# Performance work log

Hardware: AMD Instinct MI355X
Metric: run time of the kernel (lower is better)

## Reference

```python
import jax, jax.numpy as jnp
import numpy as np

B, S, U = 64, 64, 16
EMB = 10
D = U - 2 + 2 * EMB      # encoder d_model = 34
DD = 3                   # decoder d_model
FF = 4                   # dim_feedforward
NL = 4                   # num layers (enc and dec)
ENH = 2                  # encoder heads
WV, SV = 10000, 400      # word / syllable vocab sizes


def _ln(x, w, b, eps=1e-5):
    mu = jnp.mean(x, -1, keepdims=True)
    var = jnp.mean((x - mu) ** 2, -1, keepdims=True)
    return (x - mu) / jnp.sqrt(var + eps) * w + b


def _mha(xq, xkv, qkv_w, qkv_b, out_w, out_b, nhead, mask=None):
    d = xq.shape[-1]
    wq, wk, wv = jnp.split(qkv_w, 3, axis=0)
    bq, bk, bv = jnp.split(qkv_b, 3, axis=0)
    q = xq @ wq.T + bq
    k = xkv @ wk.T + bk
    v = xkv @ wv.T + bv
    b_, sq, sk = q.shape[0], q.shape[1], k.shape[1]
    dh = d // nhead
    q = q.reshape(b_, sq, nhead, dh)
    k = k.reshape(b_, sk, nhead, dh)
    v = v.reshape(b_, sk, nhead, dh)
    scores = jnp.einsum('bqhd,bkhd->bhqk', q, k) * (1.0 / np.sqrt(dh))
    if mask is not None:
        scores = scores + mask
    attn = jax.nn.softmax(scores, axis=-1)
    out = jnp.einsum('bhqk,bkhd->bqhd', attn, v).reshape(b_, sq, d)
    return out @ out_w.T + out_b


def _pos_encoding(batch, d_model):
    # Faithful to the original quirk: pe has shape [max_len, 1, d] and is added
    # to a batch-first [B,S,D] tensor as x + pe[:B]  ->  row b of pe is added
    # to ALL sequence positions of batch element b.
    pos = jnp.arange(batch, dtype=jnp.float32)[:, None]
    div = jnp.exp(jnp.arange(0, d_model, 2, dtype=jnp.float32) * (-np.log(10000.0) / d_model))
    ang = pos * div  # [B, D/2]
    pe = jnp.stack([jnp.sin(ang), jnp.cos(ang)], axis=-1).reshape(batch, d_model)
    return pe[:, None, :]  # [B,1,D]


def setup_inputs() -> dict:
    key = jax.random.key(0)
    ks = iter(jax.random.split(key, 64))

    def n(shape, s=0.1):
        return jax.random.normal(next(ks), shape, dtype=jnp.float32) * s

    base = jax.random.uniform(next(ks), (B, S, U), dtype=jnp.float32)
    widx = jax.random.randint(next(ks), (B, S), 0, WV).astype(jnp.float32)
    sidx = jax.random.randint(next(ks), (B, S), 0, SV).astype(jnp.float32)
    src = base.at[:, :, U - 2].set(widx).at[:, :, U - 1].set(sidx)
    return {
        'src': src,
        'word_emb': jax.random.uniform(next(ks), (WV, EMB), jnp.float32, -0.1, 0.1),
        'syll_emb': jax.random.uniform(next(ks), (SV, EMB), jnp.float32, -0.1, 0.1),
        'enc_qkv_w': n((NL, 3 * D, D)), 'enc_qkv_b': jnp.zeros((NL, 3 * D)),
        'enc_out_w': n((NL, D, D)), 'enc_out_b': jnp.zeros((NL, D)),
        'enc_ln1_w': jnp.ones((NL, D)), 'enc_ln1_b': jnp.zeros((NL, D)),
        'enc_lin1_w': n((NL, FF, D)), 'enc_lin1_b': jnp.zeros((NL, FF)),
        'enc_lin2_w': n((NL, D, FF)), 'enc_lin2_b': jnp.zeros((NL, D)),
        'enc_ln2_w': jnp.ones((NL, D)), 'enc_ln2_b': jnp.zeros((NL, D)),
        'norm_w': jnp.ones((D,)), 'norm_b': jnp.zeros((D,)),
        'eo_w': jax.random.uniform(next(ks), (DD, D), jnp.float32, -0.1, 0.1),
        'eo_b': jnp.zeros((DD,)),
        'dec_sa_qkv_w': n((NL, 3 * DD, DD)), 'dec_sa_qkv_b': jnp.zeros((NL, 3 * DD)),
        'dec_sa_out_w': n((NL, DD, DD)), 'dec_sa_out_b': jnp.zeros((NL, DD)),
        'dec_ln1_w': jnp.ones((NL, DD)), 'dec_ln1_b': jnp.zeros((NL, DD)),
        'dec_ca_qkv_w': n((NL, 3 * DD, DD)), 'dec_ca_qkv_b': jnp.zeros((NL, 3 * DD)),
        'dec_ca_out_w': n((NL, DD, DD)), 'dec_ca_out_b': jnp.zeros((NL, DD)),
        'dec_ln2_w': jnp.ones((NL, DD)), 'dec_ln2_b': jnp.zeros((NL, DD)),
        'dec_lin1_w': n((NL, FF, DD)), 'dec_lin1_b': jnp.zeros((NL, FF)),
        'dec_lin2_w': n((NL, DD, FF)), 'dec_lin2_b': jnp.zeros((NL, DD)),
        'dec_ln3_w': jnp.ones((NL, DD)), 'dec_ln3_b': jnp.zeros((NL, DD)),
    }


def reference(src, word_emb, syll_emb,
              enc_qkv_w, enc_qkv_b, enc_out_w, enc_out_b,
              enc_ln1_w, enc_ln1_b, enc_lin1_w, enc_lin1_b,
              enc_lin2_w, enc_lin2_b, enc_ln2_w, enc_ln2_b,
              norm_w, norm_b, eo_w, eo_b,
              dec_sa_qkv_w, dec_sa_qkv_b, dec_sa_out_w, dec_sa_out_b,
              dec_ln1_w, dec_ln1_b,
              dec_ca_qkv_w, dec_ca_qkv_b, dec_ca_out_w, dec_ca_out_b,
              dec_ln2_w, dec_ln2_b,
              dec_lin1_w, dec_lin1_b, dec_lin2_w, dec_lin2_b,
              dec_ln3_w, dec_ln3_b):
    b, s = src.shape[0], src.shape[1]
    # embed_lyrics
    widx = src[:, :, U - 2].astype(jnp.int32)
    sidx = src[:, :, U - 1].astype(jnp.int32)
    x = jnp.concatenate([src[:, :, :U - 2], word_emb[widx], syll_emb[sidx]], axis=2)  # [B,S,D]
    x = x + _pos_encoding(b, D)
    # TransformerEncoder (post-norm, relu, dropout=0) + final LayerNorm
    for l in range(NL):
        sa = _mha(x, x, enc_qkv_w[l], enc_qkv_b[l], enc_out_w[l], enc_out_b[l], ENH)
        x = _ln(x + sa, enc_ln1_w[l], enc_ln1_b[l])
        ff = jax.nn.relu(x @ enc_lin1_w[l].T + enc_lin1_b[l]) @ enc_lin2_w[l].T + enc_lin2_b[l]
        x = _ln(x + ff, enc_ln2_w[l], enc_ln2_b[l])
    x = _ln(x, norm_w, norm_b)
    memory = x @ eo_w.T + eo_b  # [B,S,3]

    causal = jnp.where(jnp.tril(jnp.ones((s, s), bool)), 0.0, -1e9).astype(jnp.float32)

    def decode(tgt):
        y = tgt
        for l in range(NL):
            sa = _mha(y, y, dec_sa_qkv_w[l], dec_sa_qkv_b[l], dec_sa_out_w[l], dec_sa_out_b[l], 1, causal)
            y = _ln(y + sa, dec_ln1_w[l], dec_ln1_b[l])
            ca = _mha(y, memory, dec_ca_qkv_w[l], dec_ca_qkv_b[l], dec_ca_out_w[l], dec_ca_out_b[l], 1)
            y = _ln(y + ca, dec_ln2_w[l], dec_ln2_b[l])
            ff = jax.nn.relu(y @ dec_lin1_w[l].T + dec_lin1_b[l]) @ dec_lin2_w[l].T + dec_lin2_b[l]
            y = _ln(y + ff, dec_ln3_w[l], dec_ln3_b[l])
        return y

    # mask, position i only depends on tgt[:, :i+1], so a fixed-size padded
    # buffer + scan computes identical values.
    def step(tgt, i):
        out_i = jax.lax.dynamic_slice_in_dim(decode(tgt), i, 1, axis=1)  # [B,1,3]
        return jax.lax.dynamic_update_slice(tgt, out_i, (0, i + 1, 0)), None

    tgt0 = jnp.zeros((b, s, DD), jnp.float32)
    tgt, _ = jax.lax.scan(step, tgt0, jnp.arange(s - 1))
    return jnp.concatenate([tgt, src[:, :, U - 2:U - 1], src[:, :, U - 1:U]], axis=2)
```

## Files before the change

kernel.cpp:

```cpp
#include <hip/hip_runtime.h>
#include <math.h>

#define B_ 64
#define S_ 64
#define U_ 16
#define EMB_ 10
#define D_ 34
#define DD_ 3
#define FF_ 4
#define NL_ 4

typedef float v2f __attribute__((ext_vector_type(2)));

__global__ __launch_bounds__(512) void enc_kernel(
    const float* __restrict__ src, const float* __restrict__ wemb,
    const float* __restrict__ semb,
    const float* __restrict__ qkv_w, const float* __restrict__ qkv_b,
    const float* __restrict__ out_w, const float* __restrict__ out_b,
    const float* __restrict__ ln1_w, const float* __restrict__ ln1_b,
    const float* __restrict__ lin1_w, const float* __restrict__ lin1_b,
    const float* __restrict__ lin2_w, const float* __restrict__ lin2_b,
    const float* __restrict__ ln2_w, const float* __restrict__ ln2_b,
    const float* __restrict__ norm_w, const float* __restrict__ norm_b,
    const float* __restrict__ eo_w, const float* __restrict__ eo_b,
    float* __restrict__ mem, float* __restrict__ out)
{
    const int b = blockIdx.x;
    const int tid = threadIdx.x;
    const int wv_ = tid >> 6;
    const int lane = tid & 63;

    __shared__ float xs[S_][D_ + 1];
    __shared__ float tmp[S_][D_ + 1];
    __shared__ float att[S_][D_ + 1];
    __shared__ __align__(16) float qsh[2][S_][21];
    __shared__ __align__(16) float ksh[2][S_][20];
    __shared__ __align__(16) float vsh[2][S_][20];
    __shared__ float ffh[S_][5];
    __shared__ float pacc[4][128][19];

    const float rs17 = 0.24253562503633297f;
    const float negln = -logf(10000.0f) / (float)D_;

    #pragma unroll
    for (int rr = 0; rr < 5; ++rr) {
        int idx = tid + rr * 512;
        if (idx < S_ * D_) {
            int pos = idx / D_, d = idx % D_;
            float v;
            if (d < U_ - 2) {
                v = src[(b * S_ + pos) * U_ + d];
            } else if (d < U_ - 2 + EMB_) {
                int wi = (int)src[(b * S_ + pos) * U_ + (U_ - 2)];
                v = wemb[wi * EMB_ + (d - (U_ - 2))];
            } else {
                int si = (int)src[(b * S_ + pos) * U_ + (U_ - 1)];
                v = semb[si * EMB_ + (d - (U_ - 2 + EMB_))];
            }
            int k = d >> 1;
            float div = __expf((float)(2 * k) * negln);
            float ang = (float)b * div;
            v += (d & 1) ? __cosf(ang) : __sinf(ang);
            xs[pos][d] = v;
        }
    }
    __syncthreads();

    for (int l = 0; l < NL_; ++l) {
        const float* Wq = qkv_w + l * 3 * D_ * D_;
        const float* Bq = qkv_b + l * 3 * D_;

        {
            v2f xr2[17];
            #pragma unroll
            for (int d2 = 0; d2 < 17; ++d2) {
                v2f t; t.x = xs[lane][2 * d2]; t.y = xs[lane][2 * d2 + 1];
                xr2[d2] = t;
            }
            #pragma unroll
            for (int rb = 0; rb < 13; ++rb) {
                int r = wv_ + (rb << 3);
                if (r < 3 * D_) {
                    int ru = __builtin_amdgcn_readfirstlane(r);
                    const v2f* w2 = (const v2f*)(Wq + ru * D_);
                    v2f a2; a2.x = Bq[ru]; a2.y = 0.f;
                    #pragma unroll
                    for (int d2 = 0; d2 < 17; ++d2)
                        a2 = __builtin_elementwise_fma(xr2[d2], w2[d2], a2);
                    float acc = a2.x + a2.y;
                    if (ru < D_)          { int h = (ru >= 17), dd = ru - h * 17; qsh[h][lane][dd] = acc; }
                    else if (ru < 2 * D_) { int rr2 = ru - D_;     int h = (rr2 >= 17), dd = rr2 - h * 17; ksh[h][lane][dd] = acc; }
                    else                  { int rr2 = ru - 2 * D_; int h = (rr2 >= 17), dd = rr2 - h * 17; vsh[h][lane][dd] = acc; }
                }
            }
        }
        __syncthreads();

        {
            int c = tid >> 7, hq = tid & 127;
            int h = hq >> 6, qi = hq & 63;
            float qv[17], acc[17];
            #pragma unroll
            for (int d = 0; d < 17; ++d) { qv[d] = qsh[h][qi][d]; acc[d] = 0.f; }
            float ssum = 0.f;
            int j0 = c * 16;
            #pragma unroll 4
            for (int jj = 0; jj < 16; ++jj) {
                int j = j0 + jj;
                const float4* kr = (const float4*)ksh[h][j];
                const float4* vr = (const float4*)vsh[h][j];
                float4 k0 = kr[0], k1 = kr[1], k2 = kr[2], k3 = kr[3];
                float  k16 = ksh[h][j][16];
                float4 v0 = vr[0], v1 = vr[1], v2 = vr[2], v3 = vr[3];
                float  v16 = vsh[h][j][16];
                float sE = qv[0]*k0.x + qv[2]*k0.z + qv[4]*k1.x + qv[6]*k1.z +
                           qv[8]*k2.x + qv[10]*k2.z + qv[12]*k3.x + qv[14]*k3.z;
                float sO = qv[1]*k0.y + qv[3]*k0.w + qv[5]*k1.y + qv[7]*k1.w +
                           qv[9]*k2.y + qv[11]*k2.w + qv[13]*k3.y + qv[15]*k3.w;
                float sc = sE + sO + qv[16]*k16;
                float e = __expf(sc * rs17);
                ssum += e;
                acc[0] += e*v0.x;  acc[1] += e*v0.y;  acc[2] += e*v0.z;  acc[3] += e*v0.w;
                acc[4] += e*v1.x;  acc[5] += e*v1.y;  acc[6] += e*v1.z;  acc[7] += e*v1.w;
                acc[8] += e*v2.x;  acc[9] += e*v2.y;  acc[10] += e*v2.z; acc[11] += e*v2.w;
                acc[12] += e*v3.x; acc[13] += e*v3.y; acc[14] += e*v3.z; acc[15] += e*v3.w;
                acc[16] += e*v16;
            }
            #pragma unroll
            for (int d = 0; d < 17; ++d) pacc[c][hq][d] = acc[d];
            pacc[c][hq][17] = ssum;
        }
        __syncthreads();

        if (tid < 128) {
            int h = tid >> 6, qi = tid & 63;
            int off = h * 17;
            float ssum = pacc[0][tid][17] + pacc[1][tid][17] +
                         pacc[2][tid][17] + pacc[3][tid][17];
            float inv = 1.f / ssum;
            #pragma unroll
            for (int d = 0; d < 17; ++d)
                att[qi][off + d] = (pacc[0][tid][d] + pacc[1][tid][d] +
                                    pacc[2][tid][d] + pacc[3][tid][d]) * inv;
        }
        __syncthreads();

        {
            v2f ar2[17];
            #pragma unroll
            for (int d2 = 0; d2 < 17; ++d2) {
                v2f t; t.x = att[lane][2 * d2]; t.y = att[lane][2 * d2 + 1];
                ar2[d2] = t;
            }
            const float* Wo = out_w + l * D_ * D_;
            const float* Bo = out_b + l * D_;
            #pragma unroll
            for (int rb = 0; rb < 5; ++rb) {
                int d = wv_ + (rb << 3);
                if (d < D_) {
                    int du = __builtin_amdgcn_readfirstlane(d);
                    const v2f* w2 = (const v2f*)(Wo + du * D_);
                    v2f a2; a2.x = Bo[du]; a2.y = 0.f;
                    #pragma unroll
                    for (int d2 = 0; d2 < 17; ++d2)
                        a2 = __builtin_elementwise_fma(ar2[d2], w2[d2], a2);
                    tmp[lane][du] = xs[lane][du] + a2.x + a2.y;
                }
            }
        }
        __syncthreads();

        {
            int row = tid >> 3, sub = tid & 7;
            float s = 0.f, sq = 0.f;
            #pragma unroll
            for (int d = sub; d < D_; d += 8) { float t = tmp[row][d]; s += t; sq = fmaf(t, t, sq); }
            #pragma unroll
            for (int m = 1; m < 8; m <<= 1) { s += __shfl_xor(s, m, 8); sq += __shfl_xor(sq, m, 8); }
            float mu = s * (1.0f / D_);
            float var = fmaf(sq, 1.0f / D_, -mu * mu);
            float rstd = rsqrtf(var + 1e-5f);
            #pragma unroll
            for (int d = sub; d < D_; d += 8)
                xs[row][d] = (tmp[row][d] - mu) * rstd * ln1_w[l * D_ + d] + ln1_b[l * D_ + d];
        }
        __syncthreads();

        if (wv_ < 4) {
            int fu = __builtin_amdgcn_readfirstlane(wv_);
            const v2f* w2 = (const v2f*)(lin1_w + l * FF_ * D_ + fu * D_);
            v2f a2; a2.x = lin1_b[l * FF_ + fu]; a2.y = 0.f;
            #pragma unroll
            for (int d2 = 0; d2 < 17; ++d2) {
                v2f t; t.x = xs[lane][2 * d2]; t.y = xs[lane][2 * d2 + 1];
                a2 = __builtin_elementwise_fma(t, w2[d2], a2);
            }
            ffh[lane][fu] = fmaxf(a2.x + a2.y, 0.f);
        }
        __syncthreads();

        {
            float h0 = ffh[lane][0], h1 = ffh[lane][1],
                  h2 = ffh[lane][2], h3 = ffh[lane][3];
            const float* W2 = lin2_w + l * D_ * FF_;
            const float* B2 = lin2_b + l * D_;
            #pragma unroll
            for (int rb = 0; rb < 5; ++rb) {
                int d = wv_ + (rb << 3);
                if (d < D_) {
                    int du = __builtin_amdgcn_readfirstlane(d);
                    const float* wrow = W2 + du * FF_;
                    float acc = fmaf(h0, wrow[0], fmaf(h1, wrow[1],
                                fmaf(h2, wrow[2], fmaf(h3, wrow[3], B2[du]))));
                    tmp[lane][du] = xs[lane][du] + acc;
                }
            }
        }
        __syncthreads();

        {
            int row = tid >> 3, sub = tid & 7;
            float s = 0.f, sq = 0.f;
            #pragma unroll
            for (int d = sub; d < D_; d += 8) { float t = tmp[row][d]; s += t; sq = fmaf(t, t, sq); }
            #pragma unroll
            for (int m = 1; m < 8; m <<= 1) { s += __shfl_xor(s, m, 8); sq += __shfl_xor(sq, m, 8); }
            float mu = s * (1.0f / D_);
            float var = fmaf(sq, 1.0f / D_, -mu * mu);
            float rstd = rsqrtf(var + 1e-5f);
            #pragma unroll
            for (int d = sub; d < D_; d += 8)
                xs[row][d] = (tmp[row][d] - mu) * rstd * ln2_w[l * D_ + d] + ln2_b[l * D_ + d];
        }
        __syncthreads();
    }

    {
        int row = tid >> 3, sub = tid & 7;
        float s = 0.f, sq = 0.f;
        #pragma unroll
        for (int d = sub; d < D_; d += 8) { float t = xs[row][d]; s += t; sq = fmaf(t, t, sq); }
        #pragma unroll
        for (int m = 1; m < 8; m <<= 1) { s += __shfl_xor(s, m, 8); sq += __shfl_xor(sq, m, 8); }
        float mu = s * (1.0f / D_);
        float var = fmaf(sq, 1.0f / D_, -mu * mu);
        float rstd = rsqrtf(var + 1e-5f);
        #pragma unroll
        for (int d = sub; d < D_; d += 8)
            tmp[row][d] = (xs[row][d] - mu) * rstd * norm_w[d] + norm_b[d];
    }
    __syncthreads();

    if (wv_ < 3) {
        int ru = __builtin_amdgcn_readfirstlane(wv_);
        const v2f* w2 = (const v2f*)(eo_w + ru * D_);
        v2f a2; a2.x = eo_b[ru]; a2.y = 0.f;
        #pragma unroll
        for (int d2 = 0; d2 < 17; ++d2) {
            v2f t; t.x = tmp[lane][2 * d2]; t.y = tmp[lane][2 * d2 + 1];
            a2 = __builtin_elementwise_fma(t, w2[d2], a2);
        }
        mem[(b * S_ + lane) * DD_ + ru] = a2.x + a2.y;
    }

    if (tid < S_) {
        out[(b * S_ + tid) * 5 + 3] = src[(b * S_ + tid) * U_ + (U_ - 2)];
        out[(b * S_ + tid) * 5 + 4] = src[(b * S_ + tid) * U_ + (U_ - 1)];
    }
}

#define PIN(x) asm volatile("" : "+v"(x))

template <int N> struct IC { static constexpr int value = N; };

template <int CTRL>
__device__ __forceinline__ float dpp_add(float v) {
    int t = __builtin_amdgcn_update_dpp(0, __float_as_int(v), CTRL, 0xf, 0xf, true);
    return v + __int_as_float(t);
}

__device__ __forceinline__ float red16(float v) {
    v = dpp_add<0x111>(v);
    v = dpp_add<0x112>(v);
    v = dpp_add<0x114>(v);
    v = dpp_add<0x118>(v);
    return v;
}

template <int L>
__device__ __forceinline__ float rlane(float v) {
    return __int_as_float(__builtin_amdgcn_readlane(__float_as_int(v), L));
}

__device__ __forceinline__ void ln3e(float z0, float z1, float z2,
                                     float w0, float w1, float w2,
                                     float b0, float b1, float b2,
                                     float& o0, float& o1, float& o2) {
    float s1 = (z0 + z1) + z2;
    float s2 = fmaf(z0, z0, fmaf(z1, z1, z2 * z2));
    float mu = s1 * (1.0f / 3.0f);
    float vpe = fmaf(s2, (1.0f / 3.0f), fmaf(-mu, mu, 1e-5f));
    float rstd = __builtin_amdgcn_rsqf(vpe);
    o0 = fmaf(z0 - mu, rstd * w0, b0);
    o1 = fmaf(z1 - mu, rstd * w1, b1);
    o2 = fmaf(z2 - mu, rstd * w2, b2);
}

__global__ __launch_bounds__(64, 1) void dec_kernel(
    const float* __restrict__ mem,
    const float* __restrict__ sa_qkv_w, const float* __restrict__ sa_qkv_b,
    const float* __restrict__ sa_out_w, const float* __restrict__ sa_out_b,
    const float* __restrict__ gln1_w, const float* __restrict__ gln1_b,
    const float* __restrict__ ca_qkv_w, const float* __restrict__ ca_qkv_b,
    const float* __restrict__ ca_out_w, const float* __restrict__ ca_out_b,
    const float* __restrict__ gln2_w, const float* __restrict__ gln2_b,
    const float* __restrict__ l1_w, const float* __restrict__ l1_b,
    const float* __restrict__ l2_w, const float* __restrict__ l2_b,
    const float* __restrict__ gln3_w, const float* __restrict__ gln3_b,
    float* __restrict__ out)
{
    const int b = blockIdx.x;
    const int lane = threadIdx.x;
    const float LOG2E = 1.4426950408889634f;
    const float rs3 = 0.5773502691896258f;
    const float QS = rs3 * LOG2E;

    __shared__ __align__(16) float fst[NL_][40];
    for (int t = lane; t < NL_ * 40; t += 64) {
        int l = t / 40, s = t % 40;
        float v = 0.f;
        if      (s < 12) v = l1_w[l * 12 + s] * gln2_w[l * 3 + (s % 3)];
        else if (s < 16) {
            int j = s - 12;
            v = l1_w[l * 12 + j * 3 + 0] * gln2_b[l * 3 + 0] +
                l1_w[l * 12 + j * 3 + 1] * gln2_b[l * 3 + 1] +
                l1_w[l * 12 + j * 3 + 2] * gln2_b[l * 3 + 2] + l1_b[l * 4 + j];
        }
        else if (s < 28) v = l2_w[l * 12 + (s - 16)];
        else if (s < 31) v = l2_b[l * 3 + (s - 28)];
        else if (s < 34) v = gln3_w[l * 3 + (s - 31)];
        else if (s < 37) v = gln3_b[l * 3 + (s - 34)];
        fst[l][s] = v;
    }
    __syncthreads();

    float Wsq[NL_][9][3], Bsq[NL_][9];
    float Wso[NL_][3][3], Bso[NL_][3];
    float N1w[NL_][3], N1b[NL_][3];
    float N2w[NL_][3], N2b[NL_][3];
    float Bco[NL_][3];
    float wcu[NL_][3];
    float swcu[NL_];
    float cbb[NL_];
    float cvp[NL_][3];

    #pragma unroll
    for (int l = 0; l < NL_; ++l) {
        #pragma unroll
        for (int r = 0; r < 9; ++r) {
            float sc = (r < 3) ? QS : 1.0f;
            Bsq[l][r] = sa_qkv_b[l * 9 + r] * sc;
            #pragma unroll
            for (int c = 0; c < 3; ++c) Wsq[l][r][c] = sa_qkv_w[l * 27 + r * 3 + c] * sc;
        }
        #pragma unroll
        for (int r = 0; r < 3; ++r) {
            Bso[l][r] = sa_out_b[l * 3 + r];
            Bco[l][r] = ca_out_b[l * 3 + r];
            N1w[l][r] = gln1_w[l * 3 + r];  N1b[l][r] = gln1_b[l * 3 + r];
            N2w[l][r] = gln2_w[l * 3 + r];  N2b[l][r] = gln2_b[l * 3 + r];
            #pragma unroll
            for (int c = 0; c < 3; ++c) Wso[l][r][c] = sa_out_w[l * 9 + r * 3 + c];
        }
    }

    float m0 = mem[(b * S_ + lane) * DD_ + 0];
    float m1 = mem[(b * S_ + lane) * DD_ + 1];
    float m2 = mem[(b * S_ + lane) * DD_ + 2];

    #pragma unroll
    for (int l = 0; l < NL_; ++l) {
        float ck[3], cv[3], cuv[3];
        #pragma unroll
        for (int r = 0; r < 3; ++r) {
            ck[r] = ca_qkv_w[l * 27 + (3 + r) * 3 + 0] * m0 +
                    ca_qkv_w[l * 27 + (3 + r) * 3 + 1] * m1 +
                    ca_qkv_w[l * 27 + (3 + r) * 3 + 2] * m2 + ca_qkv_b[l * 9 + 3 + r];
            cv[r] = ca_qkv_w[l * 27 + (6 + r) * 3 + 0] * m0 +
                    ca_qkv_w[l * 27 + (6 + r) * 3 + 1] * m1 +
                    ca_qkv_w[l * 27 + (6 + r) * 3 + 2] * m2 + ca_qkv_b[l * 9 + 6 + r];
        }
        #pragma unroll
        for (int s = 0; s < 3; ++s)
            cuv[s] = QS * (ca_qkv_w[l * 27 + 0 + s] * ck[0] +
                           ca_qkv_w[l * 27 + 3 + s] * ck[1] +
                           ca_qkv_w[l * 27 + 6 + s] * ck[2]);
        float cbv = QS * (ca_qkv_b[l * 9 + 0] * ck[0] +
                          ca_qkv_b[l * 9 + 1] * ck[1] +
                          ca_qkv_b[l * 9 + 2] * ck[2]);
        #pragma unroll
        for (int r = 0; r < 3; ++r)
            cvp[l][r] = ca_out_w[l * 9 + r * 3 + 0] * cv[0] +
                        ca_out_w[l * 9 + r * 3 + 1] * cv[1] +
                        ca_out_w[l * 9 + r * 3 + 2] * cv[2];
        #pragma unroll
        for (int r = 0; r < 3; ++r) wcu[l][r] = cuv[r] * N1w[l][r];
        swcu[l] = wcu[l][0] + wcu[l][1] + wcu[l][2];
        cbb[l]  = cbv + cuv[0] * N1b[l][0] + cuv[1] * N1b[l][1] + cuv[2] * N1b[l][2];
    }

    #pragma unroll
    for (int l = 0; l < NL_; ++l) {
        #pragma unroll
        for (int r = 0; r < 9; ++r) {
            PIN(Bsq[l][r]);
            #pragma unroll
            for (int c = 0; c < 3; ++c) PIN(Wsq[l][r][c]);
        }
        PIN(swcu[l]); PIN(cbb[l]);
        #pragma unroll
        for (int r = 0; r < 3; ++r) {
            PIN(Bso[l][r]); PIN(Bco[l][r]);
            PIN(N1w[l][r]); PIN(N1b[l][r]); PIN(N2w[l][r]); PIN(N2b[l][r]);
            PIN(wcu[l][r]); PIN(cvp[l][r]);
            #pragma unroll
            for (int c = 0; c < 3; ++c) PIN(Wso[l][r][c]);
        }
    }

    float sk[NL_][3] = {{0.f}}, sv[NL_][3] = {{0.f}};

    if (lane < 3) out[(b * S_ + 0) * 5 + lane] = 0.f;

    float y0 = 0.f, y1 = 0.f, y2 = 0.f;

    auto run_range = [&](int ibeg, int iend, auto nstc) {
        constexpr int NST = decltype(nstc)::value;
        constexpr int RL = (NST == 4) ? 15 : (NST == 5) ? 31 : 63;
        for (int i = ibeg; i < iend; ++i) {
            float msa = (lane <= i) ? 0.f : -1.0e30f;
            bool isme = (lane == i);
            #pragma unroll
            for (int l = 0; l < NL_; ++l) {
                float wv[40];
                {
                    const float4* fp = (const float4*)fst[l];
                    #pragma unroll
                    for (int k = 0; k < 10; ++k) {
                        float4 t4 = fp[k];
                        wv[4 * k + 0] = t4.x; wv[4 * k + 1] = t4.y;
                        wv[4 * k + 2] = t4.z; wv[4 * k + 3] = t4.w;
                    }
                }

                float q[3], kn[3], vn[3], vp[3];
                #pragma unroll
                for (int r = 0; r < 3; ++r) {
                    kn[r] = fmaf(Wsq[l][3 + r][0], y0, fmaf(Wsq[l][3 + r][1], y1, fmaf(Wsq[l][3 + r][2], y2, Bsq[l][3 + r])));
                    q[r]  = fmaf(Wsq[l][r][0], y0, fmaf(Wsq[l][r][1], y1, fmaf(Wsq[l][r][2], y2, Bsq[l][r])));
                    vn[r] = fmaf(Wsq[l][6 + r][0], y0, fmaf(Wsq[l][6 + r][1], y1, fmaf(Wsq[l][6 + r][2], y2, Bsq[l][6 + r])));
                }
                #pragma unroll
                for (int r = 0; r < 3; ++r)
                    vp[r] = fmaf(Wso[l][r][0], vn[0], fmaf(Wso[l][r][1], vn[1], Wso[l][r][2] * vn[2]));
                if (isme) {
                    #pragma unroll
                    for (int r = 0; r < 3; ++r) { sk[l][r] = kn[r]; sv[l][r] = vp[r]; }
                }
                float sc = fmaf(q[0], sk[l][0], fmaf(q[1], sk[l][1], fmaf(q[2], sk[l][2], msa)));
                float e = __builtin_amdgcn_exp2f(sc);
                float se  = red16(e);
                float sa0 = red16(e * sv[l][0]);
                float sa1 = red16(e * sv[l][1]);
                float sa2 = red16(e * sv[l][2]);
                if constexpr (NST >= 5) {
                    se  = dpp_add<0x142>(se);  sa0 = dpp_add<0x142>(sa0);
                    sa1 = dpp_add<0x142>(sa1); sa2 = dpp_add<0x142>(sa2);
                }
                if constexpr (NST >= 6) {
                    se  = dpp_add<0x143>(se);  sa0 = dpp_add<0x143>(sa0);
                    sa1 = dpp_add<0x143>(sa1); sa2 = dpp_add<0x143>(sa2);
                }
                float yb0 = y0 + Bso[l][0], yb1 = y1 + Bso[l][1], yb2 = y2 + Bso[l][2];
                float es = rlane<RL>(se);
                float S0 = rlane<RL>(sa0), S1 = rlane<RL>(sa1), S2 = rlane<RL>(sa2);
                float inv = __builtin_amdgcn_rcpf(es);
                float z0 = fmaf(S0, inv, yb0), z1 = fmaf(S1, inv, yb1), z2v = fmaf(S2, inv, yb2);

                float s1m = (z0 + z1) + z2v;
                float mu = s1m * (1.0f / 3.0f);
                float zw = fmaf(z0, wcu[l][0], fmaf(z1, wcu[l][1], z2v * wcu[l][2]));
                float inner = fmaf(-mu, swcu[l], zw);
                float s2m = fmaf(z0, z0, fmaf(z1, z1, z2v * z2v));
                float vpe = fmaf(s2m, (1.0f / 3.0f), fmaf(-mu, mu, 1e-5f));
                float rstd1 = __builtin_amdgcn_rsqf(vpe);
                float sc2 = fmaf(rstd1, inner, cbb[l]);
                float e2 = __builtin_amdgcn_exp2f(sc2);
                float ce  = red16(e2);
                float ca0 = red16(e2 * cvp[l][0]);
                float ca1 = red16(e2 * cvp[l][1]);
                float ca2 = red16(e2 * cvp[l][2]);
                ce  = dpp_add<0x142>(ce);  ca0 = dpp_add<0x142>(ca0);
                ca1 = dpp_add<0x142>(ca1); ca2 = dpp_add<0x142>(ca2);
                ce  = dpp_add<0x143>(ce);  ca0 = dpp_add<0x143>(ca0);
                ca1 = dpp_add<0x143>(ca1); ca2 = dpp_add<0x143>(ca2);
                float y1_0 = fmaf(z0 - mu, rstd1 * N1w[l][0], N1b[l][0]);
                float y1_1 = fmaf(z1 - mu, rstd1 * N1w[l][1], N1b[l][1]);
                float y1_2 = fmaf(z2v - mu, rstd1 * N1w[l][2], N1b[l][2]);
                float yc0 = y1_0 + Bco[l][0], yc1 = y1_1 + Bco[l][1], yc2 = y1_2 + Bco[l][2];
                float cs = rlane<63>(ce);
                float C0 = rlane<63>(ca0), C1 = rlane<63>(ca1), C2 = rlane<63>(ca2);
                float inv2 = __builtin_amdgcn_rcpf(cs);
                float g0 = fmaf(C0, inv2, yc0), g1 = fmaf(C1, inv2, yc1), g2 = fmaf(C2, inv2, yc2);

                float t1m = (g0 + g1) + g2;
                float mu2 = t1m * (1.0f / 3.0f);
                float c20 = g0 - mu2, c21 = g1 - mu2, c22 = g2 - mu2;
                float t2m = fmaf(g0, g0, fmaf(g1, g1, g2 * g2));
                float vpe2 = fmaf(t2m, (1.0f / 3.0f), fmaf(-mu2, mu2, 1e-5f));
                float rstd2 = __builtin_amdgcn_rsqf(vpe2);
                #pragma unroll
                for (int k = 0; k < 37; ++k) PIN(wv[k]);
                float d0 = fmaf(wv[0], c20, fmaf(wv[1],  c21, wv[2]  * c22));
                float d1 = fmaf(wv[3], c20, fmaf(wv[4],  c21, wv[5]  * c22));
                float d2 = fmaf(wv[6], c20, fmaf(wv[7],  c21, wv[8]  * c22));
                float d3 = fmaf(wv[9], c20, fmaf(wv[10], c21, wv[11] * c22));
                float h0 = fmaxf(fmaf(rstd2, d0, wv[12]), 0.f);
                float h1 = fmaxf(fmaf(rstd2, d1, wv[13]), 0.f);
                float h2 = fmaxf(fmaf(rstd2, d2, wv[14]), 0.f);
                float h3 = fmaxf(fmaf(rstd2, d3, wv[15]), 0.f);
                float y2_0 = fmaf(c20, rstd2 * N2w[l][0], N2b[l][0]);
                float y2_1 = fmaf(c21, rstd2 * N2w[l][1], N2b[l][1]);
                float y2_2 = fmaf(c22, rstd2 * N2w[l][2], N2b[l][2]);
                float yf0 = y2_0 + wv[28], yf1 = y2_1 + wv[29], yf2 = y2_2 + wv[30];
                float f0 = fmaf(wv[16], h0, fmaf(wv[17], h1, fmaf(wv[18], h2, fmaf(wv[19], h3, yf0))));
                float f1 = fmaf(wv[20], h0, fmaf(wv[21], h1, fmaf(wv[22], h2, fmaf(wv[23], h3, yf1))));
                float f2 = fmaf(wv[24], h0, fmaf(wv[25], h1, fmaf(wv[26], h2, fmaf(wv[27], h3, yf2))));
                ln3e(f0, f1, f2,
                     wv[31], wv[32], wv[33], wv[34], wv[35], wv[36],
                     y0, y1, y2);
            }
            if (lane == 0) {
                out[(b * S_ + i + 1) * 5 + 0] = y0;
                out[(b * S_ + i + 1) * 5 + 1] = y1;
                out[(b * S_ + i + 1) * 5 + 2] = y2;
            }
        }
    };

    run_range(0, 15, IC<4>{});
    run_range(15, 31, IC<5>{});
    run_range(31, S_ - 1, IC<6>{});
}

extern "C" void kernel_launch(void* const* d_in, const int* in_sizes, int n_in,
                              void* d_out, int out_size, void* d_ws, size_t ws_size,
                              hipStream_t stream) {
    const float* src  = (const float*)d_in[0];
    const float* wemb = (const float*)d_in[1];
    const float* semb = (const float*)d_in[2];

    float* mem = (float*)d_ws;
    float* out = (float*)d_out;

    enc_kernel<<<B_, 512, 0, stream>>>(
        src, wemb, semb,
        (const float*)d_in[3],  (const float*)d_in[4],
        (const float*)d_in[5],  (const float*)d_in[6],
        (const float*)d_in[7],  (const float*)d_in[8],
        (const float*)d_in[9],  (const float*)d_in[10],
        (const float*)d_in[11], (const float*)d_in[12],
        (const float*)d_in[13], (const float*)d_in[14],
        (const float*)d_in[15], (const float*)d_in[16],
        (const float*)d_in[17], (const float*)d_in[18],
        mem, out);

    dec_kernel<<<B_, 64, 0, stream>>>(
        mem,
        (const float*)d_in[19], (const float*)d_in[20],
        (const float*)d_in[21], (const float*)d_in[22],
        (const float*)d_in[23], (const float*)d_in[24],
        (const float*)d_in[25], (const float*)d_in[26],
        (const float*)d_in[27], (const float*)d_in[28],
        (const float*)d_in[29], (const float*)d_in[30],
        (const float*)d_in[31], (const float*)d_in[32],
        (const float*)d_in[33], (const float*)d_in[34],
        (const float*)d_in[35], (const float*)d_in[36],
        out);
}
```

Measured before the change: 316.2 us.

## Interleave two batch elements per decoder wave with butterfly reductions and rcp-free softmax

Each decoder wave now processes two batch elements at once, interleaving their serial dependency chains to hide latency, and the grid is halved. Lane reductions switch from row-shift DPP plus readlane to a full butterfly (DPP, permlane16/32 swap) so every lane holds the sum. The softmax normalisation is folded into the layer norm by scaling the residual by the sum and scaling epsilon by its square, which removes the reciprocal. The fixed-range prefix reductions are replaced by full 64-lane reductions every step, and register pressure doubles.

Result: slower. 517.3 us (+63.6%).

```diff
diff --git a/kernel.cpp b/kernel.cpp
--- a/kernel.cpp
+++ b/kernel.cpp
@@ -11,6 +11,7 @@
 #define NL_ 4
 
 typedef float v2f __attribute__((ext_vector_type(2)));
+typedef unsigned uint2v __attribute__((ext_vector_type(2)));
 
 __global__ __launch_bounds__(512) void enc_kernel(
     const float* __restrict__ src, const float* __restrict__ wemb,
@@ -271,25 +272,37 @@
 
 #define PIN(x) asm volatile("" : "+v"(x))
 
-template <int N> struct IC { static constexpr int value = N; };
-
 template <int CTRL>
 __device__ __forceinline__ float dpp_add(float v) {
     int t = __builtin_amdgcn_update_dpp(0, __float_as_int(v), CTRL, 0xf, 0xf, true);
     return v + __int_as_float(t);
 }
 
-__device__ __forceinline__ float red16(float v) {
-    v = dpp_add<0x111>(v);
-    v = dpp_add<0x112>(v);
-    v = dpp_add<0x114>(v);
-    v = dpp_add<0x118>(v);
+__device__ __forceinline__ float bfly_sum(float v) {
+    v = dpp_add<0xB1>(v);
+    v = dpp_add<0x4E>(v);
+    v = dpp_add<0x124>(v);
+    v = dpp_add<0x128>(v);
+#if __has_builtin(__builtin_amdgcn_permlane16_swap)
+    {
+        uint2v p = __builtin_amdgcn_permlane16_swap(__float_as_uint(v), __float_as_uint(v), false, false);
+        v = __uint_as_float(p.x) + __uint_as_float(p.y);
+    }
+#else
+    v += __uint_as_float(__builtin_amdgcn_ds_swizzle(__float_as_int(v), 0x401F));
+#endif
+#if __has_builtin(__builtin_amdgcn_permlane32_swap)
+    {
+        uint2v p = __builtin_amdgcn_permlane32_swap(__float_as_uint(v), __float_as_uint(v), false, false);
+        v = __uint_as_float(p.x) + __uint_as_float(p.y);
+    }
+#else
+    {
+        int ix = (((int)threadIdx.x & 63) ^ 32) << 2;
+        v += __uint_as_float(__builtin_amdgcn_ds_bpermute(ix, __float_as_int(v)));
+    }
+#endif
     return v;
-}
-
-template <int L>
-__device__ __forceinline__ float rlane(float v) {
-    return __int_as_float(__builtin_amdgcn_readlane(__float_as_int(v), L));
 }
 
 __device__ __forceinline__ void ln3e(float z0, float z1, float z2,
@@ -319,7 +332,7 @@
     const float* __restrict__ gln3_w, const float* __restrict__ gln3_b,
     float* __restrict__ out)
 {
-    const int b = blockIdx.x;
+    const int b0 = blockIdx.x * 2;
     const int lane = threadIdx.x;
     const float LOG2E = 1.4426950408889634f;
     const float rs3 = 0.5773502691896258f;
@@ -349,10 +362,10 @@
     float N1w[NL_][3], N1b[NL_][3];
     float N2w[NL_][3], N2b[NL_][3];
     float Bco[NL_][3];
-    float wcu[NL_][3];
-    float swcu[NL_];
-    float cbb[NL_];
-    float cvp[NL_][3];
+    float wcu[2][NL_][3];
+    float swcu[2][NL_];
+    float cbb[2][NL_];
+    float cvp[2][NL_][3];
 
     #pragma unroll
     for (int l = 0; l < NL_; ++l) {
@@ -374,84 +387,95 @@
         }
     }
 
-    float m0 = mem[(b * S_ + lane) * DD_ + 0];
-    float m1 = mem[(b * S_ + lane) * DD_ + 1];
-    float m2 = mem[(b * S_ + lane) * DD_ + 2];
+    #pragma unroll
+    for (int u = 0; u < 2; ++u) {
+        int bb = b0 + u;
+        float m0 = mem[(bb * S_ + lane) * DD_ + 0];
+        float m1 = mem[(bb * S_ + lane) * DD_ + 1];
+        float m2 = mem[(bb * S_ + lane) * DD_ + 2];
+        #pragma unroll
+        for (int l = 0; l < NL_; ++l) {
+            float ck[3], cv[3], cuv[3];
+            #pragma unroll
+            for (int r = 0; r < 3; ++r) {
+                ck[r] = ca_qkv_w[l * 27 + (3 + r) * 3 + 0] * m0 +
+                        ca_qkv_w[l * 27 + (3 + r) * 3 + 1] * m1 +
+                        ca_qkv_w[l * 27 + (3 + r) * 3 + 2] * m2 + ca_qkv_b[l * 9 + 3 + r];
+                cv[r] = ca_qkv_w[l * 27 + (6 + r) * 3 + 0] * m0 +
+                        ca_qkv_w[l * 27 + (6 + r) * 3 + 1] * m1 +
+                        ca_qkv_w[l * 27 + (6 + r) * 3 + 2] * m2 + ca_qkv_b[l * 9 + 6 + r];
+            }
+            #pragma unroll
+            for (int s = 0; s < 3; ++s)
+                cuv[s] = QS * (ca_qkv_w[l * 27 + 0 + s] * ck[0] +
+                               ca_qkv_w[l * 27 + 3 + s] * ck[1] +
+                               ca_qkv_w[l * 27 + 6 + s] * ck[2]);
+            float cbv = QS * (ca_qkv_b[l * 9 + 0] * ck[0] +
+                              ca_qkv_b[l * 9 + 1] * ck[1] +
+                              ca_qkv_b[l * 9 + 2] * ck[2]);
+            #pragma unroll
+            for (int r = 0; r < 3; ++r)
+                cvp[u][l][r] = ca_out_w[l * 9 + r * 3 + 0] * cv[0] +
+                               ca_out_w[l * 9 + r * 3 + 1] * cv[1] +
+                               ca_out_w[l * 9 + r * 3 + 2] * cv[2];
+            #pragma unroll
+            for (int r = 0; r < 3; ++r) wcu[u][l][r] = cuv[r] * N1w[l][r];
+            swcu[u][l] = wcu[u][l][0] + wcu[u][l][1] + wcu[u][l][2];
+            cbb[u][l]  = cbv + cuv[0] * N1b[l][0] + cuv[1] * N1b[l][1] + cuv[2] * N1b[l][2];
+        }
+    }
 
     #pragma unroll
     for (int l = 0; l < NL_; ++l) {
-        float ck[3], cv[3], cuv[3];
-        #pragma unroll
-        for (int r = 0; r < 3; ++r) {
-            ck[r] = ca_qkv_w[l * 27 + (3 + r) * 3 + 0] * m0 +
-                    ca_qkv_w[l * 27 + (3 + r) * 3 + 1] * m1 +
-                    ca_qkv_w[l * 27 + (3 + r) * 3 + 2] * m2 + ca_qkv_b[l * 9 + 3 + r];
-            cv[r] = ca_qkv_w[l * 27 + (6 + r) * 3 + 0] * m0 +
-                    ca_qkv_w[l * 27 + (6 + r) * 3 + 1] * m1 +
-                    ca_qkv_w[l * 27 + (6 + r) * 3 + 2] * m2 + ca_qkv_b[l * 9 + 6 + r];
-        }
-        #pragma unroll
-        for (int s = 0; s < 3; ++s)
-            cuv[s] = QS * (ca_qkv_w[l * 27 + 0 + s] * ck[0] +
-                           ca_qkv_w[l * 27 + 3 + s] * ck[1] +
-                           ca_qkv_w[l * 27 + 6 + s] * ck[2]);
-        float cbv = QS * (ca_qkv_b[l * 9 + 0] * ck[0] +
-                          ca_qkv_b[l * 9 + 1] * ck[1] +
-                          ca_qkv_b[l * 9 + 2] * ck[2]);
-        #pragma unroll
-        for (int r = 0; r < 3; ++r)
-            cvp[l][r] = ca_out_w[l * 9 + r * 3 + 0] * cv[0] +
-                        ca_out_w[l * 9 + r * 3 + 1] * cv[1] +
-                        ca_out_w[l * 9 + r * 3 + 2] * cv[2];
-        #pragma unroll
-        for (int r = 0; r < 3; ++r) wcu[l][r] = cuv[r] * N1w[l][r];
-        swcu[l] = wcu[l][0] + wcu[l][1] + wcu[l][2];
-        cbb[l]  = cbv + cuv[0] * N1b[l][0] + cuv[1] * N1b[l][1] + cuv[2] * N1b[l][2];
-    }
-
-    #pragma unroll
-    for (int l = 0; l < NL_; ++l) {
         #pragma unroll
         for (int r = 0; r < 9; ++r) {
             PIN(Bsq[l][r]);
             #pragma unroll
             for (int c = 0; c < 3; ++c) PIN(Wsq[l][r][c]);
         }
-        PIN(swcu[l]); PIN(cbb[l]);
         #pragma unroll
         for (int r = 0; r < 3; ++r) {
             PIN(Bso[l][r]); PIN(Bco[l][r]);
             PIN(N1w[l][r]); PIN(N1b[l][r]); PIN(N2w[l][r]); PIN(N2b[l][r]);
-            PIN(wcu[l][r]); PIN(cvp[l][r]);
             #pragma unroll
             for (int c = 0; c < 3; ++c) PIN(Wso[l][r][c]);
         }
-    }
-
-    float sk[NL_][3] = {{0.f}}, sv[NL_][3] = {{0.f}};
-
-    if (lane < 3) out[(b * S_ + 0) * 5 + lane] = 0.f;
-
-    float y0 = 0.f, y1 = 0.f, y2 = 0.f;
-
-    auto run_range = [&](int ibeg, int iend, auto nstc) {
-        constexpr int NST = decltype(nstc)::value;
-        constexpr int RL = (NST == 4) ? 15 : (NST == 5) ? 31 : 63;
-        for (int i = ibeg; i < iend; ++i) {
-            float msa = (lane <= i) ? 0.f : -1.0e30f;
-            bool isme = (lane == i);
-            #pragma unroll
-            for (int l = 0; l < NL_; ++l) {
-                float wv[40];
-                {
-                    const float4* fp = (const float4*)fst[l];
-                    #pragma unroll
-                    for (int k = 0; k < 10; ++k) {
-                        float4 t4 = fp[k];
-                        wv[4 * k + 0] = t4.x; wv[4 * k + 1] = t4.y;
-                        wv[4 * k + 2] = t4.z; wv[4 * k + 3] = t4.w;
-                    }
-                }
+        #pragma unroll
+        for (int u = 0; u < 2; ++u) {
+            PIN(swcu[u][l]); PIN(cbb[u][l]);
+            #pragma unroll
+            for (int r = 0; r < 3; ++r) { PIN(wcu[u][l][r]); PIN(cvp[u][l][r]); }
+        }
+    }
+
+    float sk[2][NL_][3] = {{{0.f}}}, sv[2][NL_][3] = {{{0.f}}};
+
+    if (lane < 3) {
+        out[(b0 * S_ + 0) * 5 + lane] = 0.f;
+        out[((b0 + 1) * S_ + 0) * 5 + lane] = 0.f;
+    }
+
+    float y[2][3] = {{0.f, 0.f, 0.f}, {0.f, 0.f, 0.f}};
+
+    for (int i = 0; i < S_ - 1; ++i) {
+        float msa = (lane <= i) ? 0.f : -1.0e30f;
+        bool isme = (lane == i);
+        #pragma unroll
+        for (int l = 0; l < NL_; ++l) {
+            float wv[40];
+            {
+                const float4* fp = (const float4*)fst[l];
+                #pragma unroll
+                for (int k = 0; k < 10; ++k) {
+                    float4 t4 = fp[k];
+                    wv[4 * k + 0] = t4.x; wv[4 * k + 1] = t4.y;
+                    wv[4 * k + 2] = t4.z; wv[4 * k + 3] = t4.w;
+                }
+            }
+
+            #pragma unroll
+            for (int u = 0; u < 2; ++u) {
+                float y0 = y[u][0], y1 = y[u][1], y2 = y[u][2];
 
                 float q[3], kn[3], vn[3], vp[3];
                 #pragma unroll
@@ -465,62 +489,48 @@
                     vp[r] = fmaf(Wso[l][r][0], vn[0], fmaf(Wso[l][r][1], vn[1], Wso[l][r][2] * vn[2]));
                 if (isme) {
                     #pragma unroll
-                    for (int r = 0; r < 3; ++r) { sk[l][r] = kn[r]; sv[l][r] = vp[r]; }
-                }
-                float sc = fmaf(q[0], sk[l][0], fmaf(q[1], sk[l][1], fmaf(q[2], sk[l][2], msa)));
+                    for (int r = 0; r < 3; ++r) { sk[u][l][r] = kn[r]; sv[u][l][r] = vp[r]; }
+                }
+                float sc = fmaf(q[0], sk[u][l][0], fmaf(q[1], sk[u][l][1], fmaf(q[2], sk[u][l][2], msa)));
                 float e = __builtin_amdgcn_exp2f(sc);
-                float se  = red16(e);
-                float sa0 = red16(e * sv[l][0]);
-                float sa1 = red16(e * sv[l][1]);
-                float sa2 = red16(e * sv[l][2]);
-                if constexpr (NST >= 5) {
-                    se  = dpp_add<0x142>(se);  sa0 = dpp_add<0x142>(sa0);
-                    sa1 = dpp_add<0x142>(sa1); sa2 = dpp_add<0x142>(sa2);
-                }
-                if constexpr (NST >= 6) {
-                    se  = dpp_add<0x143>(se);  sa0 = dpp_add<0x143>(sa0);
-                    sa1 = dpp_add<0x143>(sa1); sa2 = dpp_add<0x143>(sa2);
-                }
+                float es  = bfly_sum(e);
+                float S0 = bfly_sum(e * sv[u][l][0]);
+                float S1 = bfly_sum(e * sv[u][l][1]);
+                float S2 = bfly_sum(e * sv[u][l][2]);
                 float yb0 = y0 + Bso[l][0], yb1 = y1 + Bso[l][1], yb2 = y2 + Bso[l][2];
-                float es = rlane<RL>(se);
-                float S0 = rlane<RL>(sa0), S1 = rlane<RL>(sa1), S2 = rlane<RL>(sa2);
-                float inv = __builtin_amdgcn_rcpf(es);
-                float z0 = fmaf(S0, inv, yb0), z1 = fmaf(S1, inv, yb1), z2v = fmaf(S2, inv, yb2);
+                float z0 = fmaf(yb0, es, S0), z1 = fmaf(yb1, es, S1), z2v = fmaf(yb2, es, S2);
+                float ee = es * es;
 
                 float s1m = (z0 + z1) + z2v;
                 float mu = s1m * (1.0f / 3.0f);
-                float zw = fmaf(z0, wcu[l][0], fmaf(z1, wcu[l][1], z2v * wcu[l][2]));
-                float inner = fmaf(-mu, swcu[l], zw);
+                float zw = fmaf(z0, wcu[u][l][0], fmaf(z1, wcu[u][l][1], z2v * wcu[u][l][2]));
+                float inner = fmaf(-mu, swcu[u][l], zw);
                 float s2m = fmaf(z0, z0, fmaf(z1, z1, z2v * z2v));
-                float vpe = fmaf(s2m, (1.0f / 3.0f), fmaf(-mu, mu, 1e-5f));
+                float vpe = fmaf(s2m, (1.0f / 3.0f), fmaf(-mu, mu, 1e-5f * ee));
                 float rstd1 = __builtin_amdgcn_rsqf(vpe);
-                float sc2 = fmaf(rstd1, inner, cbb[l]);
+                float sc2 = fmaf(rstd1, inner, cbb[u][l]);
                 float e2 = __builtin_amdgcn_exp2f(sc2);
-                float ce  = red16(e2);
-                float ca0 = red16(e2 * cvp[l][0]);
-                float ca1 = red16(e2 * cvp[l][1]);
-                float ca2 = red16(e2 * cvp[l][2]);
-                ce  = dpp_add<0x142>(ce);  ca0 = dpp_add<0x142>(ca0);
-                ca1 = dpp_add<0x142>(ca1); ca2 = dpp_add<0x142>(ca2);
-                ce  = dpp_add<0x143>(ce);  ca0 = dpp_add<0x143>(ca0);
-                ca1 = dpp_add<0x143>(ca1); ca2 = dpp_add<0x143>(ca2);
+                float ce = bfly_sum(e2);
+                float C0 = bfly_sum(e2 * cvp[u][l][0]);
+                float C1 = bfly_sum(e2 * cvp[u][l][1]);
+                float C2 = bfly_sum(e2 * cvp[u][l][2]);
                 float y1_0 = fmaf(z0 - mu, rstd1 * N1w[l][0], N1b[l][0]);
                 float y1_1 = fmaf(z1 - mu, rstd1 * N1w[l][1], N1b[l][1]);
                 float y1_2 = fmaf(z2v - mu, rstd1 * N1w[l][2], N1b[l][2]);
                 float yc0 = y1_0 + Bco[l][0], yc1 = y1_1 + Bco[l][1], yc2 = y1_2 + Bco[l][2];
-                float cs = rlane<63>(ce);
-                float C0 = rlane<63>(ca0), C1 = rlane<63>(ca1), C2 = rlane<63>(ca2);
-                float inv2 = __builtin_amdgcn_rcpf(cs);
-                float g0 = fmaf(C0, inv2, yc0), g1 = fmaf(C1, inv2, yc1), g2 = fmaf(C2, inv2, yc2);
+                float g0 = fmaf(yc0, ce, C0), g1 = fmaf(yc1, ce, C1), g2 = fmaf(yc2, ce, C2);
+                float cee = ce * ce;
 
                 float t1m = (g0 + g1) + g2;
                 float mu2 = t1m * (1.0f / 3.0f);
                 float c20 = g0 - mu2, c21 = g1 - mu2, c22 = g2 - mu2;
                 float t2m = fmaf(g0, g0, fmaf(g1, g1, g2 * g2));
-                float vpe2 = fmaf(t2m, (1.0f / 3.0f), fmaf(-mu2, mu2, 1e-5f));
+                float vpe2 = fmaf(t2m, (1.0f / 3.0f), fmaf(-mu2, mu2, 1e-5f * cee));
                 float rstd2 = __builtin_amdgcn_rsqf(vpe2);
-                #pragma unroll
-                for (int k = 0; k < 37; ++k) PIN(wv[k]);
+                if (u == 0) {
+                    #pragma unroll
+                    for (int k = 0; k < 37; ++k) PIN(wv[k]);
+                }
                 float d0 = fmaf(wv[0], c20, fmaf(wv[1],  c21, wv[2]  * c22));
                 float d1 = fmaf(wv[3], c20, fmaf(wv[4],  c21, wv[5]  * c22));
                 float d2 = fmaf(wv[6], c20, fmaf(wv[7],  c21, wv[8]  * c22));
@@ -538,19 +548,18 @@
                 float f2 = fmaf(wv[24], h0, fmaf(wv[25], h1, fmaf(wv[26], h2, fmaf(wv[27], h3, yf2))));
                 ln3e(f0, f1, f2,
                      wv[31], wv[32], wv[33], wv[34], wv[35], wv[36],
-                     y0, y1, y2);
-            }
-            if (lane == 0) {
-                out[(b * S_ + i + 1) * 5 + 0] = y0;
-                out[(b * S_ + i + 1) * 5 + 1] = y1;
-                out[(b * S_ + i + 1) * 5 + 2] = y2;
-            }
-        }
-    };
-
-    run_range(0, 15, IC<4>{});
-    run_range(15, 31, IC<5>{});
-    run_range(31, S_ - 1, IC<6>{});
+                     y[u][0], y[u][1], y[u][2]);
+            }
+        }
+        if (lane == 0) {
+            out[(b0 * S_ + i + 1) * 5 + 0] = y[0][0];
+            out[(b0 * S_ + i + 1) * 5 + 1] = y[0][1];
+            out[(b0 * S_ + i + 1) * 5 + 2] = y[0][2];
+            out[((b0 + 1) * S_ + i + 1) * 5 + 0] = y[1][0];
+            out[((b0 + 1) * S_ + i + 1) * 5 + 1] = y[1][1];
+            out[((b0 + 1) * S_ + i + 1) * 5 + 2] = y[1][2];
+        }
+    }
 }
 
 extern "C" void kernel_launch(void* const* d_in, const int* in_sizes, int n_in,
@@ -575,7 +584,7 @@
         (const float*)d_in[17], (const float*)d_in[18],
         mem, out);
 
-    dec_kernel<<<B_, 64, 0, stream>>>(
+    dec_kernel<<<B_ / 2, 64, 0, stream>>>(
         mem,
         (const float*)d_in[19], (const float*)d_in[20],
         (const float*)d_in[21], (const float*)d_in[22],
```
